# Optimization experiments

Measured on AMD Instinct MI355X. Metric: run time of the kernel, lower is better.

The kernel has to match this reference:

```python
import jax, jax.numpy as jnp
import numpy as np

D_MODEL = 1024
N_HEADS = 16
D_K = D_MODEL // N_HEADS
B, T = 2, 2048


def setup_inputs() -> dict:
    key = jax.random.key(0)
    ks = jax.random.split(key, 12)
    s = 0.02
    return {
        "q": jax.random.normal(ks[0], (B, T, D_MODEL), jnp.float32),
        "k": jax.random.normal(ks[1], (B, T, D_MODEL), jnp.float32),
        "v": jax.random.normal(ks[2], (B, T, D_MODEL), jnp.float32),
        "Wq": jax.random.normal(ks[3], (D_MODEL, D_MODEL), jnp.float32) * s,
        "bq": jnp.zeros((D_MODEL,), jnp.float32),
        "Wk": jax.random.normal(ks[4], (D_MODEL, D_MODEL), jnp.float32) * s,
        "bk": jnp.zeros((D_MODEL,), jnp.float32),
        "Wv": jax.random.normal(ks[5], (D_MODEL, D_MODEL), jnp.float32) * s,
        "bv": jnp.zeros((D_MODEL,), jnp.float32),
        "Wo": jax.random.normal(ks[6], (D_MODEL, D_MODEL), jnp.float32) * s,
        "bo": jnp.zeros((D_MODEL,), jnp.float32),
        "mask": jnp.ones((B, T), jnp.int32),
        "causal": 1,
    }


def reference(q, k, v, Wq, bq, Wk, bk, Wv, bv, Wo, bo, mask, causal):
    Bq, Tq, D = q.shape
    Tk = k.shape[1]
    # projections (torch Linear: x @ W.T + b), split heads -> [B, H, T, d_k]
    qh = (q @ Wq.T + bq).reshape(Bq, Tq, N_HEADS, D_K).transpose(0, 2, 1, 3)
    kh = (k @ Wk.T + bk).reshape(Bq, Tk, N_HEADS, D_K).transpose(0, 2, 1, 3)
    vh = (v @ Wv.T + bv).reshape(Bq, Tk, N_HEADS, D_K).transpose(0, 2, 1, 3)
    scores = jnp.einsum("bhqd,bhkd->bhqk", qh, kh) / jnp.sqrt(jnp.float32(D_K))
    neg_inf = jnp.float32(-jnp.inf)
    if mask is not None:
        scores = jnp.where(mask[:, None, None, :] == 0, neg_inf, scores)
    if causal:
        causal_mask = jnp.tril(jnp.ones((Tq, Tq), jnp.float32))
        scores = jnp.where(causal_mask == 0, neg_inf, scores)
    attn = jax.nn.softmax(scores, axis=-1)
    out = jnp.einsum("bhqk,bhkd->bhqd", attn, vh)
    out = out.transpose(0, 2, 1, 3).reshape(Bq, Tq, D)
    return out @ Wo.T + bo
```

## Files before the change

kernel.cpp:

```cpp
#include <hip/hip_runtime.h>
#include <cstdint>
#include <cstddef>


typedef __bf16 bf16x8 __attribute__((ext_vector_type(8)));
typedef float f32x4 __attribute__((ext_vector_type(4)));

#define MFMA(a, b, c) __builtin_amdgcn_mfma_f32_16x16x32_bf16((a), (b), (c), 0, 0, 0)

static constexpr int D_MODEL = 1024;
static constexpr int T_ = 2048;
static constexpr int M_TOK = 4096;

__device__ __forceinline__ unsigned short f32_to_bf16(float f) {
    union { float f; uint32_t u; } v; v.f = f;
    uint32_t u = v.u;
    uint32_t r = u + 0x7fffu + ((u >> 16) & 1u);
    return (unsigned short)(r >> 16);
}
__device__ __forceinline__ unsigned f32_to_bf16_fast(float f) {
    union { float f; uint32_t u; } v; v.f = f;
    return (v.u + 0x8000u) >> 16;
}

typedef __attribute__((address_space(1))) void* as1_ptr;
typedef __attribute__((address_space(3))) void* as3_ptr;
__device__ __forceinline__ void gload_lds16(const void* g, void* l) {
    __builtin_amdgcn_global_load_lds((as1_ptr)(void*)g, (as3_ptr)l, 16, 0, 0);
}

__device__ __forceinline__ int keyperm(int k) {
    return (k & 32) | ((k & 12) << 1) | ((k & 16) >> 2) | (k & 3);
}

__global__ __launch_bounds__(256) void cvt_all(
    const float* __restrict__ q, const float* __restrict__ k,
    const float* __restrict__ v, const float* __restrict__ wq,
    const float* __restrict__ wk, const float* __restrict__ wv,
    const float* __restrict__ wo, ushort4* __restrict__ dst) {
    int i = blockIdx.x * blockDim.x + threadIdx.x;
    constexpr int R = 1 << 20;
    const float* s;
    int idx;
    if (i < 3 * R) {
        s = (i < R) ? q : (i < 2 * R) ? k : v;
        idx = i & (R - 1);
    } else {
        int j = i - 3 * R;
        int w = j >> 18;
        s = (w == 0) ? wq : (w == 1) ? wk : (w == 2) ? wv : wo;
        idx = j & ((1 << 18) - 1);
    }
    float4 f = ((const float4*)s)[idx];
    ushort4 o;
    o.x = (unsigned short)f32_to_bf16(f.x); o.y = (unsigned short)f32_to_bf16(f.y);
    o.z = (unsigned short)f32_to_bf16(f.z); o.w = (unsigned short)f32_to_bf16(f.w);
    dst[i] = o;
}

template<int MODE, int NT16>
__device__ __forceinline__ void gemm_body(
    const unsigned short* __restrict__ A, const unsigned short* __restrict__ W,
    const float* __restrict__ bias, void* __restrict__ outp,
    unsigned short* As, unsigned short* Ws, int bx, int by)
{
    constexpr bool SWAP = (MODE != 2);
    constexpr int ASZ = 128 * 64;
    constexpr int WSZ = NT16 * 32 * 64;
    const int tid = threadIdx.x;
    const int lane = tid & 63, wave = tid >> 6;
    const int wm = wave >> 1, wn = wave & 1;
    const int r16 = lane & 15, kg = lane >> 4;
    const int m_blk = by * 128, n_blk = bx * (NT16 * 32);

    const unsigned short* Ap[4]; unsigned short* Al[4];
    #pragma unroll
    for (int j = 0; j < 4; ++j) {
        int si = j * 256 + tid;
        int row = si >> 3, cg = (si & 7) ^ (row & 7);
        Ap[j] = A + (size_t)(m_blk + row) * D_MODEL + cg * 8;
        Al[j] = As + (j * 256 + wave * 64) * 8;
    }
    const unsigned short* Wp[NT16]; unsigned short* Wl[NT16];
    #pragma unroll
    for (int j = 0; j < NT16; ++j) {
        int si = j * 256 + tid;
        int row = si >> 3, cg = (si & 7) ^ (row & 7);
        Wp[j] = W + (size_t)(n_blk + row) * D_MODEL + cg * 8;
        Wl[j] = Ws + (j * 256 + wave * 64) * 8;
    }

    f32x4 acc[4][NT16];
    #pragma unroll
    for (int mt = 0; mt < 4; ++mt)
        #pragma unroll
        for (int nt = 0; nt < NT16; ++nt) acc[mt][nt] = (f32x4){0, 0, 0, 0};

    auto stage = [&](int bb, int k0) {
        #pragma unroll
        for (int j = 0; j < 4; ++j)
            gload_lds16(Ap[j] + k0, Al[j] + bb * ASZ);
        #pragma unroll
        for (int j = 0; j < NT16; ++j)
            gload_lds16(Wp[j] + k0, Wl[j] + bb * WSZ);
    };

    constexpr int NKS = D_MODEL / 64;
    stage(0, 0);
    for (int ks = 0; ks < NKS; ++ks) {
        __syncthreads();
        if (ks + 1 < NKS) stage((ks + 1) & 1, (ks + 1) * 64);
        const unsigned short* Asb = As + (ks & 1) * ASZ;
        const unsigned short* Wsb = Ws + (ks & 1) * WSZ;
        #pragma unroll
        for (int kc = 0; kc < 2; ++kc) {
            bf16x8 af[4], wf[NT16];
            #pragma unroll
            for (int mt = 0; mt < 4; ++mt) {
                int row = wm * 64 + mt * 16 + r16;
                af[mt] = *(const bf16x8*)(Asb + row * 64 + (((kc * 4 + kg) ^ (row & 7)) * 8));
            }
            #pragma unroll
            for (int nt = 0; nt < NT16; ++nt) {
                int row = wn * (NT16 * 16) + nt * 16 + r16;
                wf[nt] = *(const bf16x8*)(Wsb + row * 64 + (((kc * 4 + kg) ^ (row & 7)) * 8));
            }
            #pragma unroll
            for (int mt = 0; mt < 4; ++mt)
                #pragma unroll
                for (int nt = 0; nt < NT16; ++nt)
                    acc[mt][nt] = SWAP ? MFMA(wf[nt], af[mt], acc[mt][nt])
                                       : MFMA(af[mt], wf[nt], acc[mt][nt]);
        }
    }
    if (MODE == 2) {
        #pragma unroll
        for (int nt = 0; nt < NT16; ++nt) {
            int n = n_blk + wn * (NT16 * 16) + nt * 16 + r16;
            float bn = bias[n];
            int hh = n >> 6, dki = n & 63;
            #pragma unroll
            for (int mt = 0; mt < 4; ++mt) {
                int m0 = m_blk + wm * 64 + mt * 16 + kg * 4;
                int mp = (m0 & ~63) | keyperm(m0 & 63);
                int bb = mp >> 11, ti = mp & 2047;
                ushort4 pk;
                pk.x = f32_to_bf16(acc[mt][nt][0] + bn);
                pk.y = f32_to_bf16(acc[mt][nt][1] + bn);
                pk.z = f32_to_bf16(acc[mt][nt][2] + bn);
                pk.w = f32_to_bf16(acc[mt][nt][3] + bn);
                *(ushort4*)((unsigned short*)outp +
                    ((size_t)(bb * 16 + hh) * 64 + dki) * 2048 + ti) = pk;
            }
        }
    } else {
        #pragma unroll
        for (int nt = 0; nt < NT16; ++nt) {
            int n0 = n_blk + wn * (NT16 * 16) + nt * 16 + kg * 4;
            float4 bn4 = *(const float4*)(bias + n0);
            #pragma unroll
            for (int mt = 0; mt < 4; ++mt) {
                int m = m_blk + wm * 64 + mt * 16 + r16;
                if (MODE == 3) {
                    float4 st;
                    st.x = acc[mt][nt][0] + bn4.x; st.y = acc[mt][nt][1] + bn4.y;
                    st.z = acc[mt][nt][2] + bn4.z; st.w = acc[mt][nt][3] + bn4.w;
                    *(float4*)((float*)outp + (size_t)m * D_MODEL + n0) = st;
                } else {
                    ushort4 pk;
                    pk.x = f32_to_bf16(acc[mt][nt][0] + bn4.x);
                    pk.y = f32_to_bf16(acc[mt][nt][1] + bn4.y);
                    pk.z = f32_to_bf16(acc[mt][nt][2] + bn4.z);
                    pk.w = f32_to_bf16(acc[mt][nt][3] + bn4.w);
                    *(ushort4*)((unsigned short*)outp + (size_t)m * D_MODEL + n0) = pk;
                }
            }
        }
    }
}

__global__ __launch_bounds__(256) void gemm_qkv(
    const unsigned short* __restrict__ qb, const unsigned short* __restrict__ kb,
    const unsigned short* __restrict__ vb, const unsigned short* __restrict__ Wqb,
    const unsigned short* __restrict__ Wkb, const unsigned short* __restrict__ Wvb,
    const float* __restrict__ bq, const float* __restrict__ bk, const float* __restrict__ bv,
    unsigned short* __restrict__ Qhp, unsigned short* __restrict__ Khp,
    unsigned short* __restrict__ Vtp)
{
    __shared__ __align__(16) unsigned short As[2 * 128 * 64];
    __shared__ __align__(16) unsigned short Ws[2 * 128 * 64];
    int flat = blockIdx.x + (blockIdx.y << 3) + (blockIdx.z << 8);
    int w = (flat & 7) * 96 + (flat >> 3);
    int bx = w & 7, by = (w >> 3) & 31, z = w >> 8;
    const unsigned short* A = (z == 0) ? qb : (z == 1) ? kb : vb;
    const unsigned short* W = (z == 0) ? Wqb : (z == 1) ? Wkb : Wvb;
    const float* bias = (z == 0) ? bq : (z == 1) ? bk : bv;
    if (z < 2)
        gemm_body<0, 4>(A, W, bias, (z == 0) ? (void*)Qhp : (void*)Khp, As, Ws,
                        bx, by);
    else
        gemm_body<2, 4>(A, W, bias, (void*)Vtp, As, Ws, bx, by);
}

__global__ __launch_bounds__(256) void gemm_out(
    const unsigned short* __restrict__ ab, const unsigned short* __restrict__ Wob,
    const float* __restrict__ bo, float* __restrict__ outp)
{
    __shared__ __align__(16) unsigned short As[2 * 128 * 64];
    __shared__ __align__(16) unsigned short Ws[2 * 64 * 64];
    int flat = blockIdx.x + (blockIdx.y << 4);
    int w = (flat & 7) * 64 + (flat >> 3);
    int bx = w & 15, by = w >> 4;
    gemm_body<3, 2>(ab, Wob, bo, (void*)outp, As, Ws, bx, by);
}

__global__ __launch_bounds__(256) void attn_fwd(
    const unsigned short* __restrict__ Qh, const unsigned short* __restrict__ Kh,
    const unsigned short* __restrict__ Vt, const int* __restrict__ mask,
    const int* __restrict__ causal_p, unsigned short* __restrict__ attnout)
{
    __shared__ __align__(16) unsigned short Ks[2][64 * 64];
    __shared__ __align__(16) unsigned short Vs[2][64 * 64];
    __shared__ unsigned long long kmS[32];

    const int tid = threadIdx.x;
    const int lane = tid & 63, wave = tid >> 6;
    const int bh = blockIdx.x;
    const int y = blockIdx.y, y0 = y & 7, j4 = y >> 3;
    const int qc = (j4 == 0) ? y0 : (j4 == 1) ? (15 - y0)
                 : (j4 == 2) ? (16 + y0) : (31 - y0);
    const int b = bh >> 4, h = bh & 15;
    const int causal = *causal_p;
    const int r16 = lane & 15, kg = lane >> 4;

    const int q0 = qc * 64 + wave * 16;

    const unsigned short* Qb = Qh + (size_t)b * T_ * D_MODEL + h * 64;
    const unsigned short* Kb = Kh + (size_t)b * T_ * D_MODEL + h * 64;
    const unsigned short* Vb = Vt + (size_t)bh * 64 * T_;
    const int* mb = mask + b * T_;

    #pragma unroll
    for (int t = wave; t < 32; t += 4) {
        unsigned long long m = __ballot(mb[t * 64 + lane] != 0);
        if (lane == 0) kmS[t] = m;
    }

    bf16x8 qf0 = *(const bf16x8*)(Qb + (size_t)(q0 + r16) * D_MODEL + kg * 8);
    bf16x8 qf1 = *(const bf16x8*)(Qb + (size_t)(q0 + r16) * D_MODEL + 32 + kg * 8);

    float l = 0.f;
    f32x4 o[4];
    #pragma unroll
    for (int f = 0; f < 4; ++f) o[f] = (f32x4){0, 0, 0, 0};
    const float sc2 = 0.18033688011112042f;
    const int lim = wave * 16 + r16;

    const int nT = causal ? (qc + 1) : 32;

    auto stage = [&](int buf, int t) {
        int t0 = t * 64;
        #pragma unroll
        for (int j = 0; j < 2; ++j) {
            int si = j * 256 + tid;
            int row = si >> 3, cg = (si & 7) ^ (row & 7);
            gload_lds16(Kb + (size_t)(t0 + row) * D_MODEL + cg * 8,
                        (char*)Ks[buf] + (j * 256 + wave * 64) * 16);
            gload_lds16(Vb + (size_t)row * T_ + t0 + cg * 8,
                        (char*)Vs[buf] + (j * 256 + wave * 64) * 16);
        }
    };

    stage(0, 0);
    for (int t = 0; t < nT; ++t) {
        __syncthreads();
        if (t + 1 < nT) stage((t + 1) & 1, t + 1);
        const unsigned short* Kst = Ks[t & 1];
        const unsigned short* Vst = Vs[t & 1];
        const bool diag = causal && (t == qc);

        unsigned long long km = kmS[t];

        f32x4 s[4];
        #pragma unroll
        for (int c = 0; c < 4; ++c) {
            int key = c * 16 + r16;
            bf16x8 kf0 = *(const bf16x8*)(Kst + key * 64 + ((kg ^ (key & 7)) * 8));
            bf16x8 kf1 = *(const bf16x8*)(Kst + key * 64 + (((4 + kg) ^ (key & 7)) * 8));
            f32x4 z = (f32x4){0, 0, 0, 0};
            z = MFMA(kf0, qf0, z);
            z = MFMA(kf1, qf1, z);
            s[c] = z;
        }

        float pv[4][4];
        if (!diag && km == ~0ull) {
            #pragma unroll
            for (int c = 0; c < 4; ++c)
                #pragma unroll
                for (int r = 0; r < 4; ++r) {
                    float e = __builtin_amdgcn_exp2f(s[c][r] * sc2);
                    pv[c][r] = e; l += e;
                }
        } else {
            #pragma unroll
            for (int c = 0; c < 4; ++c) {
                unsigned mc = (unsigned)(km >> (c * 16));
                #pragma unroll
                for (int r = 0; r < 4; ++r) {
                    int kbit = kg * 4 + r;
                    bool ok = ((mc >> kbit) & 1) && (!diag || (c * 16 + kbit <= lim));
                    float e = ok ? __builtin_amdgcn_exp2f(s[c][r] * sc2) : 0.f;
                    pv[c][r] = e; l += e;
                }
            }
        }

        union pk_t { unsigned u[4]; bf16x8 v; };
        pk_t pa[2];
        #pragma unroll
        for (int c = 0; c < 4; ++c) {
            int half = (c & 1) * 2;
            pa[c >> 1].u[half]     = f32_to_bf16_fast(pv[c][0]) | (f32_to_bf16_fast(pv[c][1]) << 16);
            pa[c >> 1].u[half + 1] = f32_to_bf16_fast(pv[c][2]) | (f32_to_bf16_fast(pv[c][3]) << 16);
        }

        #pragma unroll
        for (int f = 0; f < 4; ++f) {
            int row = f * 16 + r16;
            int rx = row & 7;
            #pragma unroll
            for (int cp = 0; cp < 2; ++cp) {
                int g = cp * 4 + kg;
                bf16x8 vf = *(const bf16x8*)(Vst + row * 64 + ((g ^ rx) * 8));
                o[f] = MFMA(pa[cp].v, vf, o[f]);
            }
        }
    }

    l += __shfl_xor(l, 16, 64); l += __shfl_xor(l, 32, 64);
    float inv = (l > 0.f) ? 1.0f / l : 0.f;
    #pragma unroll
    for (int r = 0; r < 4; ++r) {
        int ql = kg * 4 + r;
        float iv = __shfl(inv, ql, 64);
        size_t base = ((size_t)(b * T_ + q0 + ql)) * D_MODEL + h * 64;
        #pragma unroll
        for (int f = 0; f < 4; ++f)
            attnout[base + f * 16 + r16] = f32_to_bf16(o[f][r] * iv);
    }
}

extern "C" void kernel_launch(void* const* d_in, const int* in_sizes, int n_in,
                              void* d_out, int out_size, void* d_ws, size_t ws_size,
                              hipStream_t stream) {
    const float* q  = (const float*)d_in[0];
    const float* k  = (const float*)d_in[1];
    const float* v  = (const float*)d_in[2];
    const float* Wq = (const float*)d_in[3];
    const float* bq = (const float*)d_in[4];
    const float* Wk = (const float*)d_in[5];
    const float* bk = (const float*)d_in[6];
    const float* Wv = (const float*)d_in[7];
    const float* bv = (const float*)d_in[8];
    const float* Wo = (const float*)d_in[9];
    const float* bo = (const float*)d_in[10];
    const int* mask   = (const int*)d_in[11];
    const int* causal = (const int*)d_in[12];

    const size_t SZ_TOK = (size_t)M_TOK * D_MODEL;
    const size_t SZ_W   = (size_t)D_MODEL * D_MODEL;

    unsigned short* qb  = (unsigned short*)d_ws;
    unsigned short* kb  = qb  + SZ_TOK;
    unsigned short* vb  = kb  + SZ_TOK;
    unsigned short* Wqb = vb  + SZ_TOK;
    unsigned short* Wkb = Wqb + SZ_W;
    unsigned short* Wvb = Wkb + SZ_W;
    unsigned short* Wob = Wvb + SZ_W;
    unsigned short* Qhp = Wob + SZ_W;
    unsigned short* Khp = Qhp + SZ_TOK;
    unsigned short* Vtp = Khp + SZ_TOK;
    unsigned short* ab  = Vtp + SZ_TOK;

    cvt_all<<<16384, 256, 0, stream>>>(q, k, v, Wq, Wk, Wv, Wo, (ushort4*)qb);

    gemm_qkv<<<dim3(D_MODEL / 128, M_TOK / 128, 3), 256, 0, stream>>>(
        qb, kb, vb, Wqb, Wkb, Wvb, bq, bk, bv, Qhp, Khp, Vtp);

    attn_fwd<<<dim3(32, 32), 256, 0, stream>>>(Qhp, Khp, Vtp, mask, causal, ab);

    gemm_out<<<dim3(D_MODEL / 64, M_TOK / 128), 256, 0, stream>>>(ab, Wob, bo,
                                                                  (float*)d_out);
}
```

Baseline: 222.9 us.

## Triple-buffer GEMM K-loop with 32-wide K tiles and explicit vmcnt waits

```diff
diff --git a/kernel.cpp b/kernel.cpp
--- a/kernel.cpp
+++ b/kernel.cpp
@@ -65,29 +65,45 @@
     unsigned short* As, unsigned short* Ws, int bx, int by)
 {
     constexpr bool SWAP = (MODE != 2);
-    constexpr int ASZ = 128 * 64;
-    constexpr int WSZ = NT16 * 32 * 64;
+    constexpr int BKE = 32;
+    constexpr int ASZ = 128 * BKE;
+    constexpr int WSZ = NT16 * 32 * BKE;
+    constexpr int AL = ASZ / (256 * 8);
+    constexpr int WL = WSZ / (256 * 8);
+    constexpr int NKS = D_MODEL / BKE;
     const int tid = threadIdx.x;
     const int lane = tid & 63, wave = tid >> 6;
     const int wm = wave >> 1, wn = wave & 1;
     const int r16 = lane & 15, kg = lane >> 4;
     const int m_blk = by * 128, n_blk = bx * (NT16 * 32);
 
-    const unsigned short* Ap[4]; unsigned short* Al[4];
-    #pragma unroll
-    for (int j = 0; j < 4; ++j) {
+    const unsigned short* Ap[AL]; unsigned short* Albase[AL];
+    #pragma unroll
+    for (int j = 0; j < AL; ++j) {
         int si = j * 256 + tid;
-        int row = si >> 3, cg = (si & 7) ^ (row & 7);
-        Ap[j] = A + (size_t)(m_blk + row) * D_MODEL + cg * 8;
-        Al[j] = As + (j * 256 + wave * 64) * 8;
-    }
-    const unsigned short* Wp[NT16]; unsigned short* Wl[NT16];
-    #pragma unroll
-    for (int j = 0; j < NT16; ++j) {
+        int row = si >> 2, p = si & 3, g = p ^ ((row >> 1) & 3);
+        Ap[j] = A + (size_t)(m_blk + row) * D_MODEL + g * 8;
+        Albase[j] = As + (j * 256 + wave * 64) * 8;
+    }
+    const unsigned short* Wp[WL]; unsigned short* Wlbase[WL];
+    #pragma unroll
+    for (int j = 0; j < WL; ++j) {
         int si = j * 256 + tid;
-        int row = si >> 3, cg = (si & 7) ^ (row & 7);
-        Wp[j] = W + (size_t)(n_blk + row) * D_MODEL + cg * 8;
-        Wl[j] = Ws + (j * 256 + wave * 64) * 8;
+        int row = si >> 2, p = si & 3, g = p ^ ((row >> 1) & 3);
+        Wp[j] = W + (size_t)(n_blk + row) * D_MODEL + g * 8;
+        Wlbase[j] = Ws + (j * 256 + wave * 64) * 8;
+    }
+
+    int aoff[4], woff[NT16];
+    #pragma unroll
+    for (int mt = 0; mt < 4; ++mt) {
+        int row = wm * 64 + mt * 16 + r16;
+        aoff[mt] = row * BKE + ((kg ^ ((row >> 1) & 3)) * 8);
+    }
+    #pragma unroll
+    for (int nt = 0; nt < NT16; ++nt) {
+        int row = wn * (NT16 * 16) + nt * 16 + r16;
+        woff[nt] = row * BKE + ((kg ^ ((row >> 1) & 3)) * 8);
     }
 
     f32x4 acc[4][NT16];
@@ -98,41 +114,43 @@
 
     auto stage = [&](int bb, int k0) {
         #pragma unroll
-        for (int j = 0; j < 4; ++j)
-            gload_lds16(Ap[j] + k0, Al[j] + bb * ASZ);
-        #pragma unroll
-        for (int j = 0; j < NT16; ++j)
-            gload_lds16(Wp[j] + k0, Wl[j] + bb * WSZ);
+        for (int j = 0; j < AL; ++j)
+            gload_lds16(Ap[j] + k0, Albase[j] + bb * ASZ);
+        #pragma unroll
+        for (int j = 0; j < WL; ++j)
+            gload_lds16(Wp[j] + k0, Wlbase[j] + bb * WSZ);
     };
 
-    constexpr int NKS = D_MODEL / 64;
     stage(0, 0);
+    stage(1, BKE);
+    int cb = 0;
     for (int ks = 0; ks < NKS; ++ks) {
-        __syncthreads();
-        if (ks + 1 < NKS) stage((ks + 1) & 1, (ks + 1) * 64);
-        const unsigned short* Asb = As + (ks & 1) * ASZ;
-        const unsigned short* Wsb = Ws + (ks & 1) * WSZ;
-        #pragma unroll
-        for (int kc = 0; kc < 2; ++kc) {
-            bf16x8 af[4], wf[NT16];
-            #pragma unroll
-            for (int mt = 0; mt < 4; ++mt) {
-                int row = wm * 64 + mt * 16 + r16;
-                af[mt] = *(const bf16x8*)(Asb + row * 64 + (((kc * 4 + kg) ^ (row & 7)) * 8));
-            }
-            #pragma unroll
-            for (int nt = 0; nt < NT16; ++nt) {
-                int row = wn * (NT16 * 16) + nt * 16 + r16;
-                wf[nt] = *(const bf16x8*)(Wsb + row * 64 + (((kc * 4 + kg) ^ (row & 7)) * 8));
-            }
-            #pragma unroll
-            for (int mt = 0; mt < 4; ++mt)
-                #pragma unroll
-                for (int nt = 0; nt < NT16; ++nt)
-                    acc[mt][nt] = SWAP ? MFMA(wf[nt], af[mt], acc[mt][nt])
-                                       : MFMA(af[mt], wf[nt], acc[mt][nt]);
-        }
-    }
+        if (ks + 1 < NKS) asm volatile("s_waitcnt vmcnt(4)" ::: "memory");
+        else              asm volatile("s_waitcnt vmcnt(0)" ::: "memory");
+        __builtin_amdgcn_s_barrier();
+        __builtin_amdgcn_sched_barrier(0);
+        if (ks + 2 < NKS) {
+            int sb = cb + 2; if (sb >= 3) sb -= 3;
+            stage(sb, (ks + 2) * BKE);
+        }
+        const unsigned short* Asb = As + cb * ASZ;
+        const unsigned short* Wsb = Ws + cb * WSZ;
+        bf16x8 af[4], wf[NT16];
+        #pragma unroll
+        for (int mt = 0; mt < 4; ++mt)
+            af[mt] = *(const bf16x8*)(Asb + aoff[mt]);
+        #pragma unroll
+        for (int nt = 0; nt < NT16; ++nt)
+            wf[nt] = *(const bf16x8*)(Wsb + woff[nt]);
+        #pragma unroll
+        for (int mt = 0; mt < 4; ++mt)
+            #pragma unroll
+            for (int nt = 0; nt < NT16; ++nt)
+                acc[mt][nt] = SWAP ? MFMA(wf[nt], af[mt], acc[mt][nt])
+                                   : MFMA(af[mt], wf[nt], acc[mt][nt]);
+        cb = (cb == 2) ? 0 : cb + 1;
+    }
+
     if (MODE == 2) {
         #pragma unroll
         for (int nt = 0; nt < NT16; ++nt) {
@@ -187,8 +205,8 @@
     unsigned short* __restrict__ Qhp, unsigned short* __restrict__ Khp,
     unsigned short* __restrict__ Vtp)
 {
-    __shared__ __align__(16) unsigned short As[2 * 128 * 64];
-    __shared__ __align__(16) unsigned short Ws[2 * 128 * 64];
+    __shared__ __align__(16) unsigned short As[3 * 128 * 32];
+    __shared__ __align__(16) unsigned short Ws[3 * 128 * 32];
     int flat = blockIdx.x + (blockIdx.y << 3) + (blockIdx.z << 8);
     int w = (flat & 7) * 96 + (flat >> 3);
     int bx = w & 7, by = (w >> 3) & 31, z = w >> 8;
@@ -206,12 +224,12 @@
     const unsigned short* __restrict__ ab, const unsigned short* __restrict__ Wob,
     const float* __restrict__ bo, float* __restrict__ outp)
 {
-    __shared__ __align__(16) unsigned short As[2 * 128 * 64];
-    __shared__ __align__(16) unsigned short Ws[2 * 64 * 64];
-    int flat = blockIdx.x + (blockIdx.y << 4);
-    int w = (flat & 7) * 64 + (flat >> 3);
-    int bx = w & 15, by = w >> 4;
-    gemm_body<3, 2>(ab, Wob, bo, (void*)outp, As, Ws, bx, by);
+    __shared__ __align__(16) unsigned short As[3 * 128 * 32];
+    __shared__ __align__(16) unsigned short Ws[3 * 128 * 32];
+    int flat = blockIdx.x + (blockIdx.y << 3);
+    int w = (flat & 7) * 32 + (flat >> 3);
+    int bx = w & 7, by = w >> 3;
+    gemm_body<3, 4>(ab, Wob, bo, (void*)outp, As, Ws, bx, by);
 }
 
 __global__ __launch_bounds__(256) void attn_fwd(
@@ -390,6 +408,6 @@
 
     attn_fwd<<<dim3(32, 32), 256, 0, stream>>>(Qhp, Khp, Vtp, mask, causal, ab);
 
-    gemm_out<<<dim3(D_MODEL / 64, M_TOK / 128), 256, 0, stream>>>(ab, Wob, bo,
-                                                                  (float*)d_out);
-}
+    gemm_out<<<dim3(D_MODEL / 128, M_TOK / 128), 256, 0, stream>>>(ab, Wob, bo,
+                                                                   (float*)d_out);
+}
```

Measured after the change: 220.8 us. No clear change (-0.9%).
